# Kernel optimization log

Hardware: AMD Instinct MI355X
Metric: run time of the kernel (lower is better)

## Reference

```python
import jax, jax.numpy as jnp
import numpy as np
from jax import lax

EPS = 1e-5  # torch LayerNorm default

def setup_inputs() -> dict:
    key = jax.random.key(0)
    ks = jax.random.split(key, 8)
    B, T = 512, 4096
    x = jax.random.normal(ks[0], (B, T, 16), dtype=jnp.float32)
    # shared causal conv: Conv1d(in=8, out=16, k=3) -> weight (O,I,K), bias (O,)
    conv_w = jax.random.normal(ks[1], (16, 8, 3), dtype=jnp.float32) * 0.2
    conv_b = jax.random.normal(ks[2], (16,), dtype=jnp.float32) * 0.05
    # dominance MLP: Linear(32,16) -> ReLU -> Linear(16,2); stored (in,out)
    w1 = jax.random.normal(ks[3], (32, 16), dtype=jnp.float32) * 0.17
    b1 = jax.random.normal(ks[4], (16,), dtype=jnp.float32) * 0.05
    w2 = jax.random.normal(ks[5], (16, 2), dtype=jnp.float32) * 0.25
    b2 = jax.random.normal(ks[6], (2,), dtype=jnp.float32) * 0.05
    ln_g = jnp.ones((16,), dtype=jnp.float32)
    ln_b = jnp.zeros((16,), dtype=jnp.float32)
    return {"x": x, "conv_w": conv_w, "conv_b": conv_b, "w1": w1, "b1": b1,
            "w2": w2, "b2": b2, "ln_g": ln_g, "ln_b": ln_b}

def reference(x, conv_w, conv_b, w1, b1, w2, b2, ln_g, ln_b):
    B = x.shape[0]
    X_L = x[:, :, :8]   # (B,T,8)
    X_R = x[:, :, 8:]   # (B,T,8)
    # shared conv applied to both arms: stack along batch for one conv call
    stacked = jnp.concatenate([X_L, X_R], axis=0).transpose(0, 2, 1)  # (2B,8,T)
    h = lax.conv_general_dilated(stacked, conv_w, window_strides=(1,),
                                 padding=[(2, 0)],  # causal left-pad for k=3
                                 dimension_numbers=("NCH", "OIH", "NCH"))
    h = jax.nn.relu(h + conv_b[None, :, None]).transpose(0, 2, 1)  # (2B,T,16)
    H_L, H_R = h[:B], h[B:]
    H_cat = jnp.concatenate([H_L, H_R], axis=-1)  # (B,T,32)
    hidden = jax.nn.relu(jnp.einsum("btf,fh->bth", H_cat, w1) + b1)
    alpha_logits = jnp.einsum("bth,hc->btc", hidden, w2) + b2  # (B,T,2)
    alphas = jax.nn.softmax(alpha_logits, axis=-1)
    tilde_X = jnp.concatenate([alphas[:, :, 0:1] * X_L,
                               alphas[:, :, 1:2] * X_R], axis=-1)
    y = x + tilde_X
    mu = jnp.mean(y, axis=-1, keepdims=True)
    var = jnp.mean(jnp.square(y - mu), axis=-1, keepdims=True)
    out_X = (y - mu) * jax.lax.rsqrt(var + EPS) * ln_g + ln_b
    return (out_X, alphas)
```

## Files before the change

kernel.cpp:

```cpp
#include <hip/hip_runtime.h>

#define BB 512
#define TT 4096
#define EPSF 1e-5f

typedef __attribute__((ext_vector_type(8))) short bf16x8;
typedef __attribute__((ext_vector_type(4))) float f32x4;

__device__ __forceinline__ unsigned short f2b(float f) {
    union { float f; unsigned u; } v; v.f = f;
    unsigned r = (v.u + 0x7fffu + ((v.u >> 16) & 1u)) >> 16;
    return (unsigned short)r;
}

#define XROWB   48
#define HROWB   80
#define HIDROWB 80
#define H_OFF   20480

__global__ __launch_bounds__(256) void bimanual_mfma_kernel(
    const float* __restrict__ x,
    const float* __restrict__ conv_w,
    const float* __restrict__ conv_b,
    const float* __restrict__ w1,
    const float* __restrict__ b1,
    const float* __restrict__ w2,
    const float* __restrict__ b2,
    const float* __restrict__ ln_g,
    const float* __restrict__ ln_b,
    float* __restrict__ out)
{
    __shared__ __align__(16) unsigned char lds[40960];

    const int tid  = threadIdx.x;
    const int lane = tid & 63;
    const int w    = tid >> 6;
    const int col  = lane & 15;
    const int g    = lane >> 4;
    const int p0   = blockIdx.x << 8;

    bf16x8 Bc, B1;
#pragma unroll
    for (int j = 0; j < 8; ++j) {
        float wc = (g < 3) ? conv_w[(col * 8 + j) * 3 + g] : 0.f;
        Bc[j] = (short)f2b(wc);
        B1[j] = (short)f2b(w1[(g * 8 + j) * 16 + col]);
    }
    const float bias_c = conv_b[col];
    const float bias_1 = b1[col];

    const bool tz = ((blockIdx.x & 15) == 0);
    for (int r = tid; r < 258; r += 256) {
        unsigned u[8];
        if (tz && r < 2) {
#pragma unroll
            for (int k = 0; k < 8; ++k) u[k] = 0u;
        } else {
            const float4* src = reinterpret_cast<const float4*>(x + (size_t)(p0 + r - 2) * 16);
            float f[16];
#pragma unroll
            for (int k = 0; k < 4; ++k) {
                float4 v = src[k];
                f[4 * k] = v.x; f[4 * k + 1] = v.y; f[4 * k + 2] = v.z; f[4 * k + 3] = v.w;
            }
#pragma unroll
            for (int k = 0; k < 8; ++k)
                u[k] = (unsigned)f2b(f[2 * k]) | ((unsigned)f2b(f[2 * k + 1]) << 16);
        }
        *reinterpret_cast<uint4*>(lds + r * XROWB)      = make_uint4(u[0], u[1], u[2], u[3]);
        *reinterpret_cast<uint4*>(lds + r * XROWB + 16) = make_uint4(u[4], u[5], u[6], u[7]);
    }
    __syncthreads();

    const bf16x8 zfrag = {0, 0, 0, 0, 0, 0, 0, 0};
#pragma unroll
    for (int m = 0; m < 4; ++m) {
        const int posm = (w << 6) + (m << 4);
        const int arow = posm + col + ((g < 3) ? g : 0);
        bf16x8 AL = *reinterpret_cast<const bf16x8*>(lds + arow * XROWB);
        bf16x8 AR = *reinterpret_cast<const bf16x8*>(lds + arow * XROWB + 16);
        if (g == 3) { AL = zfrag; AR = zfrag; }
        f32x4 accL = {bias_c, bias_c, bias_c, bias_c};
        f32x4 accR = accL;
        accL = __builtin_amdgcn_mfma_f32_16x16x32_bf16(AL, Bc, accL, 0, 0, 0);
        accR = __builtin_amdgcn_mfma_f32_16x16x32_bf16(AR, Bc, accR, 0, 0, 0);
        const int prow = posm + (g << 2);
#pragma unroll
        for (int q = 0; q < 4; ++q) {
            *reinterpret_cast<unsigned short*>(lds + H_OFF + (prow + q) * HROWB + col * 2)
                = f2b(fmaxf(accL[q], 0.f));
            *reinterpret_cast<unsigned short*>(lds + H_OFF + (prow + q) * HROWB + 32 + col * 2)
                = f2b(fmaxf(accR[q], 0.f));
        }
    }
    __syncthreads();

#pragma unroll
    for (int m = 0; m < 4; ++m) {
        const int posm = (w << 6) + (m << 4);
        bf16x8 A = *reinterpret_cast<const bf16x8*>(
            lds + H_OFF + (posm + col) * HROWB + g * 16);
        f32x4 acc = {bias_1, bias_1, bias_1, bias_1};
        acc = __builtin_amdgcn_mfma_f32_16x16x32_bf16(A, B1, acc, 0, 0, 0);
        const int prow = posm + (g << 2);
#pragma unroll
        for (int q = 0; q < 4; ++q)
            *reinterpret_cast<float*>(lds + (prow + q) * HIDROWB + col * 4) = fmaxf(acc[q], 0.f);
    }
    __syncthreads();

    float hid[16];
    const float4* hp = reinterpret_cast<const float4*>(lds + tid * HIDROWB);
#pragma unroll
    for (int k = 0; k < 4; ++k) {
        float4 v = hp[k];
        hid[4 * k] = v.x; hid[4 * k + 1] = v.y; hid[4 * k + 2] = v.z; hid[4 * k + 3] = v.w;
    }
    float l0 = b2[0], l1 = b2[1];
#pragma unroll
    for (int j = 0; j < 16; ++j) {
        l0 = fmaf(hid[j], w2[2 * j], l0);
        l1 = fmaf(hid[j], w2[2 * j + 1], l1);
    }
    const float mm = fmaxf(l0, l1);
    const float e0 = __expf(l0 - mm);
    const float e1 = __expf(l1 - mm);
    const float inv = 1.f / (e0 + e1);
    const float a0 = e0 * inv;
    const float a1 = e1 * inv;

    const size_t rowbase = (size_t)(p0 + tid) * 16;
    float xv[16];
    const float4* xp = reinterpret_cast<const float4*>(x + rowbase);
#pragma unroll
    for (int k = 0; k < 4; ++k) {
        float4 v = xp[k];
        xv[4 * k] = v.x; xv[4 * k + 1] = v.y; xv[4 * k + 2] = v.z; xv[4 * k + 3] = v.w;
    }
    float y[16];
    const float g0 = 1.f + a0;
    const float g1 = 1.f + a1;
#pragma unroll
    for (int i = 0; i < 8; ++i) y[i] = xv[i] * g0;
#pragma unroll
    for (int i = 0; i < 8; ++i) y[8 + i] = xv[8 + i] * g1;

    float s = 0.f;
#pragma unroll
    for (int i = 0; i < 16; ++i) s += y[i];
    const float mu = s * (1.f / 16.f);
    float var = 0.f;
#pragma unroll
    for (int i = 0; i < 16; ++i) {
        const float d = y[i] - mu;
        var = fmaf(d, d, var);
    }
    const float rs = rsqrtf(var * (1.f / 16.f) + EPSF);

    float4* od = reinterpret_cast<float4*>(out + rowbase);
#pragma unroll
    for (int k = 0; k < 4; ++k) {
        float o0 = fmaf((y[4 * k]     - mu) * rs, ln_g[4 * k],     ln_b[4 * k]);
        float o1 = fmaf((y[4 * k + 1] - mu) * rs, ln_g[4 * k + 1], ln_b[4 * k + 1]);
        float o2 = fmaf((y[4 * k + 2] - mu) * rs, ln_g[4 * k + 2], ln_b[4 * k + 2]);
        float o3 = fmaf((y[4 * k + 3] - mu) * rs, ln_g[4 * k + 3], ln_b[4 * k + 3]);
        od[k] = make_float4(o0, o1, o2, o3);
    }
    *reinterpret_cast<float2*>(out + (size_t)BB * TT * 16 + (size_t)(p0 + tid) * 2)
        = make_float2(a0, a1);
}

extern "C" void kernel_launch(void* const* d_in, const int* in_sizes, int n_in,
                              void* d_out, int out_size, void* d_ws, size_t ws_size,
                              hipStream_t stream) {
    const float* x      = (const float*)d_in[0];
    const float* conv_w = (const float*)d_in[1];
    const float* conv_b = (const float*)d_in[2];
    const float* w1     = (const float*)d_in[3];
    const float* b1     = (const float*)d_in[4];
    const float* w2     = (const float*)d_in[5];
    const float* b2     = (const float*)d_in[6];
    const float* ln_g   = (const float*)d_in[7];
    const float* ln_b   = (const float*)d_in[8];
    float* out = (float*)d_out;

    const int total = BB * TT;
    dim3 block(256);
    dim3 grid(total / 256);
    hipLaunchKernelGGL(bimanual_mfma_kernel, grid, block, 0, stream,
                       x, conv_w, conv_b, w1, b1, w2, b2, ln_g, ln_b, out);
}
```

Before: 275.4 us.

## Fuse conv, MLP and softmax per wave with transposed MFMA and shuffle reductions

Each thread now loads its own x row once and keeps it in registers, which removes the second global read of x. The conv and first linear layer are chained per wave through a small per-wave LDS buffer, with the MFMA operands swapped so outputs land in a layout suitable for the next stage. Two block-wide barriers are dropped, and the w2 projection is reduced with cross-lane shuffles instead of an LDS round trip. This cuts LDS usage and synchronisation, but it relies on subtle lane-to-row mappings to compute the alphas correctly.

```diff
diff --git a/kernel.cpp b/kernel.cpp
--- a/kernel.cpp
+++ b/kernel.cpp
@@ -1,4 +1,5 @@
 #include <hip/hip_runtime.h>
+#include <hip/hip_bf16.h>
 
 #define BB 512
 #define TT 4096
@@ -7,18 +8,22 @@
 typedef __attribute__((ext_vector_type(8))) short bf16x8;
 typedef __attribute__((ext_vector_type(4))) float f32x4;
 
-__device__ __forceinline__ unsigned short f2b(float f) {
-    union { float f; unsigned u; } v; v.f = f;
-    unsigned r = (v.u + 0x7fffu + ((v.u >> 16) & 1u)) >> 16;
-    return (unsigned short)r;
+__device__ __forceinline__ unsigned pkbf(float lo, float hi) {
+    __hip_bfloat162 h = __float22bfloat162_rn(make_float2(lo, hi));
+    return *reinterpret_cast<unsigned*>(&h);
+}
+__device__ __forceinline__ short b16(float f) {
+    __hip_bfloat16 h = __float2bfloat16(f);
+    return *reinterpret_cast<short*>(&h);
 }
 
-#define XROWB   48
-#define HROWB   80
-#define HIDROWB 80
-#define H_OFF   20480
+#define XPITCH 48
+#define XROWS  258
+#define XSZ    (XROWS * XPITCH)
+#define HPITCH 80
+#define LDS_SZ (XSZ + 4 * 16 * HPITCH)
 
-__global__ __launch_bounds__(256) void bimanual_mfma_kernel(
+__global__ __launch_bounds__(256) void bimanual_fused2_kernel(
     const float* __restrict__ x,
     const float* __restrict__ conv_w,
     const float* __restrict__ conv_b,
@@ -30,116 +35,108 @@
     const float* __restrict__ ln_b,
     float* __restrict__ out)
 {
-    __shared__ __align__(16) unsigned char lds[40960];
+    __shared__ __align__(16) unsigned char lds[LDS_SZ];
 
     const int tid  = threadIdx.x;
     const int lane = tid & 63;
     const int w    = tid >> 6;
-    const int col  = lane & 15;
+    const int c    = lane & 15;
     const int g    = lane >> 4;
     const int p0   = blockIdx.x << 8;
 
-    bf16x8 Bc, B1;
+    unsigned char* Hb = lds + XSZ + w * (16 * HPITCH);
+
+    bf16x8 Wc, W1;
 #pragma unroll
     for (int j = 0; j < 8; ++j) {
-        float wc = (g < 3) ? conv_w[(col * 8 + j) * 3 + g] : 0.f;
-        Bc[j] = (short)f2b(wc);
-        B1[j] = (short)f2b(w1[(g * 8 + j) * 16 + col]);
+        const float wc = (g < 3) ? conv_w[(c * 8 + j) * 3 + g] : 0.f;
+        Wc[j] = b16(wc);
+        W1[j] = b16(w1[(g * 8 + j) * 16 + c]);
     }
-    const float bias_c = conv_b[col];
-    const float bias_1 = b1[col];
+    const float4 bc4 = *reinterpret_cast<const float4*>(conv_b + 4 * g);
+    const float4 b14 = *reinterpret_cast<const float4*>(b1 + 4 * g);
+    const float4 w2a = reinterpret_cast<const float4*>(w2)[2 * g];
+    const float4 w2b = reinterpret_cast<const float4*>(w2)[2 * g + 1];
 
-    const bool tz = ((blockIdx.x & 15) == 0);
-    for (int r = tid; r < 258; r += 256) {
+    const size_t rowbase = (size_t)(p0 + tid) * 16;
+    float xv[16];
+    {
+        const float4* xp = reinterpret_cast<const float4*>(x + rowbase);
+#pragma unroll
+        for (int k = 0; k < 4; ++k) {
+            float4 v = xp[k];
+            xv[4 * k] = v.x; xv[4 * k + 1] = v.y; xv[4 * k + 2] = v.z; xv[4 * k + 3] = v.w;
+        }
         unsigned u[8];
-        if (tz && r < 2) {
+#pragma unroll
+        for (int k = 0; k < 8; ++k) u[k] = pkbf(xv[2 * k], xv[2 * k + 1]);
+        *reinterpret_cast<uint4*>(lds + (tid + 2) * XPITCH)      = make_uint4(u[0], u[1], u[2], u[3]);
+        *reinterpret_cast<uint4*>(lds + (tid + 2) * XPITCH + 16) = make_uint4(u[4], u[5], u[6], u[7]);
+    }
+    if (tid < 2) {
+        const bool tz = ((blockIdx.x & 15) == 0);
+        unsigned u[8];
+        if (tz) {
 #pragma unroll
             for (int k = 0; k < 8; ++k) u[k] = 0u;
         } else {
-            const float4* src = reinterpret_cast<const float4*>(x + (size_t)(p0 + r - 2) * 16);
+            const float4* hp = reinterpret_cast<const float4*>(x + (size_t)(p0 - 2 + tid) * 16);
             float f[16];
 #pragma unroll
             for (int k = 0; k < 4; ++k) {
-                float4 v = src[k];
+                float4 v = hp[k];
                 f[4 * k] = v.x; f[4 * k + 1] = v.y; f[4 * k + 2] = v.z; f[4 * k + 3] = v.w;
             }
 #pragma unroll
-            for (int k = 0; k < 8; ++k)
-                u[k] = (unsigned)f2b(f[2 * k]) | ((unsigned)f2b(f[2 * k + 1]) << 16);
+            for (int k = 0; k < 8; ++k) u[k] = pkbf(f[2 * k], f[2 * k + 1]);
         }
-        *reinterpret_cast<uint4*>(lds + r * XROWB)      = make_uint4(u[0], u[1], u[2], u[3]);
-        *reinterpret_cast<uint4*>(lds + r * XROWB + 16) = make_uint4(u[4], u[5], u[6], u[7]);
+        *reinterpret_cast<uint4*>(lds + tid * XPITCH)      = make_uint4(u[0], u[1], u[2], u[3]);
+        *reinterpret_cast<uint4*>(lds + tid * XPITCH + 16) = make_uint4(u[4], u[5], u[6], u[7]);
     }
     __syncthreads();
 
-    const bf16x8 zfrag = {0, 0, 0, 0, 0, 0, 0, 0};
+    const bf16x8 zf = {0, 0, 0, 0, 0, 0, 0, 0};
+    float a0own = 0.f, a1own = 0.f;
 #pragma unroll
     for (int m = 0; m < 4; ++m) {
         const int posm = (w << 6) + (m << 4);
-        const int arow = posm + col + ((g < 3) ? g : 0);
-        bf16x8 AL = *reinterpret_cast<const bf16x8*>(lds + arow * XROWB);
-        bf16x8 AR = *reinterpret_cast<const bf16x8*>(lds + arow * XROWB + 16);
-        if (g == 3) { AL = zfrag; AR = zfrag; }
-        f32x4 accL = {bias_c, bias_c, bias_c, bias_c};
+        const int arow = posm + c + ((g < 3) ? g : 0);
+        bf16x8 XL = *reinterpret_cast<const bf16x8*>(lds + arow * XPITCH);
+        bf16x8 XR = *reinterpret_cast<const bf16x8*>(lds + arow * XPITCH + 16);
+        if (g == 3) { XL = zf; XR = zf; }
+        f32x4 accL = {bc4.x, bc4.y, bc4.z, bc4.w};
         f32x4 accR = accL;
-        accL = __builtin_amdgcn_mfma_f32_16x16x32_bf16(AL, Bc, accL, 0, 0, 0);
-        accR = __builtin_amdgcn_mfma_f32_16x16x32_bf16(AR, Bc, accR, 0, 0, 0);
-        const int prow = posm + (g << 2);
-#pragma unroll
-        for (int q = 0; q < 4; ++q) {
-            *reinterpret_cast<unsigned short*>(lds + H_OFF + (prow + q) * HROWB + col * 2)
-                = f2b(fmaxf(accL[q], 0.f));
-            *reinterpret_cast<unsigned short*>(lds + H_OFF + (prow + q) * HROWB + 32 + col * 2)
-                = f2b(fmaxf(accR[q], 0.f));
+        accL = __builtin_amdgcn_mfma_f32_16x16x32_bf16(Wc, XL, accL, 0, 0, 0);
+        accR = __builtin_amdgcn_mfma_f32_16x16x32_bf16(Wc, XR, accR, 0, 0, 0);
+        const unsigned pl0 = pkbf(fmaxf(accL[0], 0.f), fmaxf(accL[1], 0.f));
+        const unsigned pl1 = pkbf(fmaxf(accL[2], 0.f), fmaxf(accL[3], 0.f));
+        const unsigned pr0 = pkbf(fmaxf(accR[0], 0.f), fmaxf(accR[1], 0.f));
+        const unsigned pr1 = pkbf(fmaxf(accR[2], 0.f), fmaxf(accR[3], 0.f));
+        *reinterpret_cast<uint2*>(Hb + c * HPITCH + g * 8)      = make_uint2(pl0, pl1);
+        *reinterpret_cast<uint2*>(Hb + c * HPITCH + 32 + g * 8) = make_uint2(pr0, pr1);
+        bf16x8 Hf = *reinterpret_cast<const bf16x8*>(Hb + c * HPITCH + g * 16);
+        f32x4 acc1 = {b14.x, b14.y, b14.z, b14.w};
+        acc1 = __builtin_amdgcn_mfma_f32_16x16x32_bf16(W1, Hf, acc1, 0, 0, 0);
+        const float h0 = fmaxf(acc1[0], 0.f), h1 = fmaxf(acc1[1], 0.f);
+        const float h2 = fmaxf(acc1[2], 0.f), h3 = fmaxf(acc1[3], 0.f);
+        float l0 = h0 * w2a.x + h1 * w2a.z + h2 * w2b.x + h3 * w2b.z;
+        float l1 = h0 * w2a.y + h1 * w2a.w + h2 * w2b.y + h3 * w2b.w;
+        l0 += __shfl_xor(l0, 16); l0 += __shfl_xor(l0, 32);
+        l1 += __shfl_xor(l1, 16); l1 += __shfl_xor(l1, 32);
+        if (g == m) {
+            l0 += b2[0]; l1 += b2[1];
+            const float mm = fmaxf(l0, l1);
+            const float e0 = __expf(l0 - mm);
+            const float e1 = __expf(l1 - mm);
+            const float inv = 1.f / (e0 + e1);
+            a0own = e0 * inv;
+            a1own = e1 * inv;
         }
     }
-    __syncthreads();
 
-#pragma unroll
-    for (int m = 0; m < 4; ++m) {
-        const int posm = (w << 6) + (m << 4);
-        bf16x8 A = *reinterpret_cast<const bf16x8*>(
-            lds + H_OFF + (posm + col) * HROWB + g * 16);
-        f32x4 acc = {bias_1, bias_1, bias_1, bias_1};
-        acc = __builtin_amdgcn_mfma_f32_16x16x32_bf16(A, B1, acc, 0, 0, 0);
-        const int prow = posm + (g << 2);
-#pragma unroll
-        for (int q = 0; q < 4; ++q)
-            *reinterpret_cast<float*>(lds + (prow + q) * HIDROWB + col * 4) = fmaxf(acc[q], 0.f);
-    }
-    __syncthreads();
-
-    float hid[16];
-    const float4* hp = reinterpret_cast<const float4*>(lds + tid * HIDROWB);
-#pragma unroll
-    for (int k = 0; k < 4; ++k) {
-        float4 v = hp[k];
-        hid[4 * k] = v.x; hid[4 * k + 1] = v.y; hid[4 * k + 2] = v.z; hid[4 * k + 3] = v.w;
-    }
-    float l0 = b2[0], l1 = b2[1];
-#pragma unroll
-    for (int j = 0; j < 16; ++j) {
-        l0 = fmaf(hid[j], w2[2 * j], l0);
-        l1 = fmaf(hid[j], w2[2 * j + 1], l1);
-    }
-    const float mm = fmaxf(l0, l1);
-    const float e0 = __expf(l0 - mm);
-    const float e1 = __expf(l1 - mm);
-    const float inv = 1.f / (e0 + e1);
-    const float a0 = e0 * inv;
-    const float a1 = e1 * inv;
-
-    const size_t rowbase = (size_t)(p0 + tid) * 16;
-    float xv[16];
-    const float4* xp = reinterpret_cast<const float4*>(x + rowbase);
-#pragma unroll
-    for (int k = 0; k < 4; ++k) {
-        float4 v = xp[k];
-        xv[4 * k] = v.x; xv[4 * k + 1] = v.y; xv[4 * k + 2] = v.z; xv[4 * k + 3] = v.w;
-    }
     float y[16];
-    const float g0 = 1.f + a0;
-    const float g1 = 1.f + a1;
+    const float g0 = 1.f + a0own;
+    const float g1 = 1.f + a1own;
 #pragma unroll
     for (int i = 0; i < 8; ++i) y[i] = xv[i] * g0;
 #pragma unroll
@@ -167,7 +164,7 @@
         od[k] = make_float4(o0, o1, o2, o3);
     }
     *reinterpret_cast<float2*>(out + (size_t)BB * TT * 16 + (size_t)(p0 + tid) * 2)
-        = make_float2(a0, a1);
+        = make_float2(a0own, a1own);
 }
 
 extern "C" void kernel_launch(void* const* d_in, const int* in_sizes, int n_in,
@@ -187,6 +184,6 @@
     const int total = BB * TT;
     dim3 block(256);
     dim3 grid(total / 256);
-    hipLaunchKernelGGL(bimanual_mfma_kernel, grid, block, 0, stream,
+    hipLaunchKernelGGL(bimanual_fused2_kernel, grid, block, 0, stream,
                        x, conv_w, conv_b, w1, b1, w2, b2, ln_g, ln_b, out);
 }
```

Measured after the change: 283.7 us. +3.0%, slower.
